# Kernel tuning notes

Measured on AMD Instinct MI355X. Metric: run time of the kernel, lower is better.

The kernel has to match this reference:

```python
import jax, jax.numpy as jnp
import numpy as np

IN_CH, OUT_CH, KS = 64, 128, 3
GRID, DEG = 8, 3
STRIDE, PAD = 1, 1
SIZE = IN_CH * KS * KS            # 576
NCOEF = GRID + DEG                # 11
GRID_RANGE = (-1.0, 1.0)


def _xavier_uniform(key, shape):
    fan_out, fan_in = shape
    a = float(np.sqrt(6.0 / (fan_in + fan_out)))
    return jax.random.uniform(key, shape, minval=-a, maxval=a, dtype=jnp.float32)


def setup_inputs() -> dict:
    key = jax.random.key(0)
    k1, k2, k3 = jax.random.split(key, 3)
    x = jax.random.normal(k1, (8, IN_CH, 32, 32), dtype=jnp.float32)
    # non-trainable knot grid, one row per unfolded feature
    knots = jnp.tile(jnp.linspace(GRID_RANGE[0], GRID_RANGE[1], GRID + 1, dtype=jnp.float32)[None, :], (SIZE, 1))
    coeff = 0.1 * jax.random.normal(k2, (OUT_CH, SIZE, NCOEF), dtype=jnp.float32)
    base_weights = _xavier_uniform(k3, (OUT_CH, SIZE))
    spline_weights = jnp.ones((OUT_CH, SIZE), dtype=jnp.float32)
    return {"x": x, "knots": knots, "coeff": coeff,
            "base_weights": base_weights, "spline_weights": spline_weights}


def bspline_basis(x, grid, k):
    # x: (S, P) evaluation points; grid: (S, G+1) knots. Returns (S, G+k, P).
    h = (grid[:, -1:] - grid[:, :1]) / (grid.shape[1] - 1)
    left = grid[:, :1] - h * jnp.arange(k, 0, -1, dtype=x.dtype)
    right = grid[:, -1:] + h * jnp.arange(1, k + 1, dtype=x.dtype)
    g = jnp.concatenate([left, grid, right], axis=1)  # (S, G+1+2k)
    xe = x[:, None, :]
    B = ((xe >= g[:, :-1, None]) & (xe < g[:, 1:, None])).astype(x.dtype)
    for d in range(1, k + 1):  # de Boor recursion over fixed degree
        B = ((xe - g[:, :-(d + 1), None]) / (g[:, d:-1, None] - g[:, :-(d + 1), None]) * B[:, :-1]
             + (g[:, d + 1:, None] - xe) / (g[:, d + 1:, None] - g[:, 1:-d, None]) * B[:, 1:])
    return B


def _unfold(x):
    # torch F.unfold with channel-major (c, kh, kw) feature ordering
    N, C, H, W = x.shape
    xp = jnp.pad(x, ((0, 0), (0, 0), (PAD, PAD), (PAD, PAD)))
    Hp = (H + 2 * PAD - KS) // STRIDE + 1
    Wp = (W + 2 * PAD - KS) // STRIDE + 1
    patches = jnp.stack([xp[:, :, i:i + STRIDE * Hp:STRIDE, j:j + STRIDE * Wp:STRIDE]
                         for i in range(KS) for j in range(KS)], axis=2)  # (N, C, KS*KS, Hp, Wp)
    L = Hp * Wp
    u = patches.reshape(N, SIZE, L)              # (N, size, L)
    u = jnp.transpose(u, (1, 0, 2)).reshape(SIZE, N * L)  # (size, N*L), col = n*L + l
    return u, Hp, Wp


def reference(x, knots, coeff, base_weights, spline_weights):
    N = x.shape[0]
    u, Hp, Wp = _unfold(x)                                   # (size, P)
    base = base_weights @ jax.nn.silu(u)                     # (Cout, P)
    B = bspline_basis(u, knots, DEG)                         # (size, ncoef, P)
    eff = spline_weights[:, :, None] * coeff                 # (Cout, size, ncoef)
    spl = jnp.einsum('csj,sjp->cp', eff, B)                  # (Cout, P)
    out = (base + spl).reshape(OUT_CH, N, Hp, Wp)
    return jnp.transpose(out, (1, 0, 2, 3))                  # (N, Cout, Hp, Wp)
```

## Files before the change

### kernel.cpp

```cpp
#include <hip/hip_runtime.h>


typedef __attribute__((ext_vector_type(8))) short bf16x8;
typedef __attribute__((ext_vector_type(4))) float f32x4;
typedef __attribute__((ext_vector_type(4))) unsigned short u16x4;

#define WSWZ_BYTES 1769472
#define PART_OFF   WSWZ_BYTES

__device__ __forceinline__ short f2bf(float f) {
    union { float f; unsigned u; } c; c.f = f;
    unsigned r = c.u + 0x7fffu + ((c.u >> 16) & 1u);
    return (short)(r >> 16);
}
__device__ __forceinline__ float bf2f(unsigned short u) {
    union { unsigned u; float f; } c; c.u = ((unsigned)u) << 16;
    return c.f;
}

__global__ void kan_weights(const float* __restrict__ coeff,
                            const float* __restrict__ basew,
                            const float* __restrict__ splw,
                            short* __restrict__ Wswz) {
    __shared__ float coeffL[6336];
    __shared__ float basewL[576];
    __shared__ float splwL[576];
    const int co = blockIdx.x;
    const int t  = threadIdx.x;
    const float* crow = coeff + co * 6336;
    for (int i = t; i < 6336; i += 256) coeffL[i] = crow[i];
    for (int i = t; i < 576; i += 256) {
        basewL[i] = basew[co * 576 + i];
        splwL[i]  = splw[co * 576 + i];
    }
    __syncthreads();
    const int cb = co >> 4, lm = co & 15;
    for (int c = t; c < 864; c += 256) {
        int kk = c >> 2, quad = c & 3;
        int f  = kk / 18;
        int rm = kk - f * 18;
        int tap = rm >> 1, ks = rm & 1;
        bf16x8 pack;
#pragma unroll
        for (int j = 0; j < 8; ++j) {
            int ci = ks * 32 + quad * 8 + j;
            int s  = ci * 9 + tap;
            float v = (f == 0) ? basewL[s] : splwL[s] * coeffL[s * 11 + (f - 1)];
            pack[j] = f2bf(v);
        }
        *(bf16x8*)(Wswz + ((kk * 8 + cb) * 64 + quad * 16 + lm) * 8) = pack;
    }
}

__global__ __launch_bounds__(256, 2)
void kan_gemm(const float* __restrict__ x,
              const short* __restrict__ Wswz,
              float* __restrict__ part) {
    __shared__ unsigned short xs[4 * 64 * 36];
    __shared__ short Bs[3 * 8704];

    const int t    = threadIdx.x;
    const int w    = t >> 6;
    const int l    = t & 63;
    const int lp   = l & 15;
    const int quad = l >> 4;
    const int wm   = w >> 1;
    const int wn   = w & 1;

    const int bz    = blockIdx.x;
    const int fg    = bz & 3;
    const int ptile = bz >> 2;
    const int n     = ptile >> 4;
    const int y0    = (ptile & 15) << 1;

#pragma unroll
    for (int it = 0; it < 8; ++it) {
        int cg = t + it * 256;
        int rr = cg >> 9, ci = (cg >> 3) & 63, q = cg & 7;
        int y  = y0 - 1 + rr;
        f32x4 v = {0.f, 0.f, 0.f, 0.f};
        if (y >= 0 && y < 32)
            v = *(const f32x4*)(x + (((n * 64 + ci) * 32 + y) * 32 + q * 4));
        u16x4 p;
        p.x = (unsigned short)f2bf(v.x); p.y = (unsigned short)f2bf(v.y);
        p.z = (unsigned short)f2bf(v.z); p.w = (unsigned short)f2bf(v.w);
        *(u16x4*)&xs[(rr * 64 + ci) * 36 + q * 4] = p;
    }
    __syncthreads();

    const int f0 = fg * 3;
    for (int it = t; it < 1088; it += 256) {
        int rr  = it / 272;
        int rem = it - rr * 272;
        int xp = rem >> 3, cch = rem & 7, c0 = cch << 3;
        bool interior = (xp >= 1 && xp <= 32);
        bf16x8 packs[3];
#pragma unroll
        for (int j = 0; j < 8; ++j) {
            float v = interior ? bf2f(xs[(rr * 64 + c0 + j) * 36 + (xp - 1)]) : 0.f;
            float silu = v / (1.f + __expf(-v));
            float tt = 4.f * v + 7.f;
            int   i0 = -100;
            float b0 = 0.f, b1 = 0.f, b2 = 0.f, b3 = 0.f;
            if (tt >= 0.f && tt < 14.f) {
                i0 = (int)tt;
                float fr  = tt - (float)i0;
                float omf = 1.f - fr;
                float fr2 = fr * fr, fr3 = fr2 * fr;
                b0 = omf * omf * omf * (1.f / 6.f);
                b1 = (3.f * fr3 - 6.f * fr2 + 4.f) * (1.f / 6.f);
                b2 = (-3.f * fr3 + 3.f * fr2 + 3.f * fr + 1.f) * (1.f / 6.f);
                b3 = fr3 * (1.f / 6.f);
            }
#pragma unroll
            for (int p = 0; p < 3; ++p) {
                int f = f0 + p;
                float val;
                if (f == 0) val = silu;
                else {
                    int jj = f - 1;
                    val = 0.f;
                    val = (jj == i0 - 3) ? b0 : val;
                    val = (jj == i0 - 2) ? b1 : val;
                    val = (jj == i0 - 1) ? b2 : val;
                    val = (jj == i0    ) ? b3 : val;
                }
                packs[p][j] = f2bf(val);
            }
        }
        int pix = rr * 34 + xp;
        int swz = (cch ^ (pix & 7)) << 3;
#pragma unroll
        for (int p = 0; p < 3; ++p)
            *(bf16x8*)&Bs[p * 8704 + pix * 64 + swz] = packs[p];
    }
    __syncthreads();

    f32x4 acc[4][2];
#pragma unroll
    for (int m = 0; m < 4; ++m)
#pragma unroll
        for (int nt = 0; nt < 2; ++nt) {
            f32x4 z = {0.f, 0.f, 0.f, 0.f};
            acc[m][nt] = z;
        }

    const short* Ap = Wswz + (size_t)(f0 * 18) * 4096 + (wm * 4) * 512 + l * 8;

    bf16x8 Abuf[4][4];
#pragma unroll
    for (int s = 0; s < 4; ++s)
#pragma unroll
        for (int m = 0; m < 4; ++m)
            Abuf[s][m] = *(const bf16x8*)(Ap + s * 4096 + m * 512);

#pragma unroll
    for (int u = 0; u < 54; ++u) {
        const int p   = u / 18;
        const int kk  = u - p * 18;
        const int tap = kk >> 1, ks = kk & 1;
        const int dy  = tap / 3;
        const int dx  = tap - dy * 3;
        const int c   = ks * 4 + quad;
        const int s   = u & 3;
        const short* B0 = Bs + p * 8704;

        bf16x8 b[2];
#pragma unroll
        for (int nt = 0; nt < 2; ++nt) {
            int pix = (wn + dy) * 34 + (nt << 4) + lp + dx;
            b[nt] = *(const bf16x8*)&B0[pix * 64 + ((c ^ (pix & 7)) << 3)];
        }
#pragma unroll
        for (int nt = 0; nt < 2; ++nt) {
            acc[0][nt] = __builtin_amdgcn_mfma_f32_16x16x32_bf16(Abuf[s][0], b[nt], acc[0][nt], 0, 0, 0);
            acc[1][nt] = __builtin_amdgcn_mfma_f32_16x16x32_bf16(Abuf[s][1], b[nt], acc[1][nt], 0, 0, 0);
            acc[2][nt] = __builtin_amdgcn_mfma_f32_16x16x32_bf16(Abuf[s][2], b[nt], acc[2][nt], 0, 0, 0);
            acc[3][nt] = __builtin_amdgcn_mfma_f32_16x16x32_bf16(Abuf[s][3], b[nt], acc[3][nt], 0, 0, 0);
        }
#pragma unroll
        for (int m = 0; m < 4; ++m)
            Abuf[s][m] = *(const bf16x8*)(Ap + (u + 4) * 4096 + m * 512);
    }

    float* dst = part + (size_t)fg * 1048576;
#pragma unroll
    for (int m = 0; m < 4; ++m)
#pragma unroll
        for (int nt = 0; nt < 2; ++nt)
#pragma unroll
            for (int r = 0; r < 4; ++r) {
                int co = wm * 64 + m * 16 + quad * 4 + r;
                int y  = y0 + wn;
                int xx = (nt << 4) + lp;
                dst[((size_t)(n * 128 + co) * 32 + y) * 32 + xx] = acc[m][nt][r];
            }
}

__global__ void kan_reduce(const float* __restrict__ part,
                           float* __restrict__ out) {
    int g = blockIdx.x * 256 + threadIdx.x;
    f32x4 a = ((const f32x4*)part)[g];
#pragma unroll
    for (int s = 1; s < 4; ++s)
        a += ((const f32x4*)(part + (size_t)s * 1048576))[g];
    ((f32x4*)out)[g] = a;
}

extern "C" void kernel_launch(void* const* d_in, const int* in_sizes, int n_in,
                              void* d_out, int out_size, void* d_ws, size_t ws_size,
                              hipStream_t stream) {
    const float* x     = (const float*)d_in[0];
    const float* coeff = (const float*)d_in[2];
    const float* basew = (const float*)d_in[3];
    const float* splw  = (const float*)d_in[4];
    float* out = (float*)d_out;

    short* Wswz = (short*)d_ws;
    float* part = (float*)((char*)d_ws + PART_OFF);

    kan_weights<<<128, 256, 0, stream>>>(coeff, basew, splw, Wswz);
    kan_gemm<<<512, 256, 0, stream>>>(x, Wswz, part);
    kan_reduce<<<1024, 256, 0, stream>>>(part, out);
}
```

Before: 107.3 us.

## Split K across warp pairs in GEMM and reduce partial sums through LDS

Each warp pair now splits the K dimension (the two channel halves of each tap) instead of the pixel rows. Every warp covers all four pixel tiles, so each loaded A fragment is reused across four N tiles and global weight loads per MFMA are halved. The software-pipelined A prefetch is removed, and the two K halves are combined through shared memory before the store. The costs are more accumulator registers, two extra barriers for the reduction, and half the warps sitting idle during the final store.

```diff
diff --git a/kernel.cpp b/kernel.cpp
--- a/kernel.cpp
+++ b/kernel.cpp
@@ -65,7 +65,7 @@
     const int lp   = l & 15;
     const int quad = l >> 4;
     const int wm   = w >> 1;
-    const int wn   = w & 1;
+    const int ksw  = w & 1;
 
     const int bz    = blockIdx.x;
     const int fg    = bz & 3;
@@ -136,65 +136,70 @@
     }
     __syncthreads();
 
-    f32x4 acc[4][2];
+    f32x4 acc[4][4];
 #pragma unroll
     for (int m = 0; m < 4; ++m)
 #pragma unroll
-        for (int nt = 0; nt < 2; ++nt) {
+        for (int nt = 0; nt < 4; ++nt) {
             f32x4 z = {0.f, 0.f, 0.f, 0.f};
             acc[m][nt] = z;
         }
 
-    const short* Ap = Wswz + (size_t)(f0 * 18) * 4096 + (wm * 4) * 512 + l * 8;
-
-    bf16x8 Abuf[4][4];
-#pragma unroll
-    for (int s = 0; s < 4; ++s)
+    const short* Abase = Wswz + (size_t)(wm * 4) * 512 + l * 8;
+    const int c = ksw * 4 + quad;
+#pragma unroll
+    for (int p = 0; p < 3; ++p) {
+        const short* B0 = Bs + p * 8704;
+#pragma unroll
+        for (int tap = 0; tap < 9; ++tap) {
+            const int kk = (f0 + p) * 18 + tap * 2 + ksw;
+            const int dy = tap / 3;
+            const int dx = tap - dy * 3;
+            const short* Ak = Abase + (size_t)kk * 4096;
+            bf16x8 a[4], b[4];
+#pragma unroll
+            for (int m = 0; m < 4; ++m)
+                a[m] = *(const bf16x8*)(Ak + m * 512);
+#pragma unroll
+            for (int nt = 0; nt < 4; ++nt) {
+                int pix = ((nt >> 1) + dy) * 34 + ((nt & 1) << 4) + lp + dx;
+                b[nt] = *(const bf16x8*)&B0[pix * 64 + ((c ^ (pix & 7)) << 3)];
+            }
+#pragma unroll
+            for (int m = 0; m < 4; ++m)
+#pragma unroll
+                for (int nt = 0; nt < 4; ++nt)
+                    acc[m][nt] = __builtin_amdgcn_mfma_f32_16x16x32_bf16(a[m], b[nt], acc[m][nt], 0, 0, 0);
+        }
+    }
+
+    __syncthreads();
+    float* red = (float*)Bs;
+    if (ksw == 1) {
 #pragma unroll
         for (int m = 0; m < 4; ++m)
-            Abuf[s][m] = *(const bf16x8*)(Ap + s * 4096 + m * 512);
-
-#pragma unroll
-    for (int u = 0; u < 54; ++u) {
-        const int p   = u / 18;
-        const int kk  = u - p * 18;
-        const int tap = kk >> 1, ks = kk & 1;
-        const int dy  = tap / 3;
-        const int dx  = tap - dy * 3;
-        const int c   = ks * 4 + quad;
-        const int s   = u & 3;
-        const short* B0 = Bs + p * 8704;
-
-        bf16x8 b[2];
-#pragma unroll
-        for (int nt = 0; nt < 2; ++nt) {
-            int pix = (wn + dy) * 34 + (nt << 4) + lp + dx;
-            b[nt] = *(const bf16x8*)&B0[pix * 64 + ((c ^ (pix & 7)) << 3)];
-        }
-#pragma unroll
-        for (int nt = 0; nt < 2; ++nt) {
-            acc[0][nt] = __builtin_amdgcn_mfma_f32_16x16x32_bf16(Abuf[s][0], b[nt], acc[0][nt], 0, 0, 0);
-            acc[1][nt] = __builtin_amdgcn_mfma_f32_16x16x32_bf16(Abuf[s][1], b[nt], acc[1][nt], 0, 0, 0);
-            acc[2][nt] = __builtin_amdgcn_mfma_f32_16x16x32_bf16(Abuf[s][2], b[nt], acc[2][nt], 0, 0, 0);
-            acc[3][nt] = __builtin_amdgcn_mfma_f32_16x16x32_bf16(Abuf[s][3], b[nt], acc[3][nt], 0, 0, 0);
-        }
+#pragma unroll
+            for (int nt = 0; nt < 4; ++nt)
+                *(f32x4*)&red[(((m * 4 + nt) * 128) + wm * 64 + l) * 4] = acc[m][nt];
+    }
+    __syncthreads();
+
+    if (ksw == 0) {
+        float* dst = part + (size_t)fg * 1048576;
 #pragma unroll
         for (int m = 0; m < 4; ++m)
-            Abuf[s][m] = *(const bf16x8*)(Ap + (u + 4) * 4096 + m * 512);
-    }
-
-    float* dst = part + (size_t)fg * 1048576;
-#pragma unroll
-    for (int m = 0; m < 4; ++m)
-#pragma unroll
-        for (int nt = 0; nt < 2; ++nt)
-#pragma unroll
-            for (int r = 0; r < 4; ++r) {
-                int co = wm * 64 + m * 16 + quad * 4 + r;
-                int y  = y0 + wn;
-                int xx = (nt << 4) + lp;
-                dst[((size_t)(n * 128 + co) * 32 + y) * 32 + xx] = acc[m][nt][r];
-            }
+#pragma unroll
+            for (int nt = 0; nt < 4; ++nt) {
+                f32x4 o = acc[m][nt] + *(const f32x4*)&red[(((m * 4 + nt) * 128) + wm * 64 + l) * 4];
+                int y  = y0 + (nt >> 1);
+                int xx = ((nt & 1) << 4) + lp;
+#pragma unroll
+                for (int r = 0; r < 4; ++r) {
+                    int co = wm * 64 + m * 16 + quad * 4 + r;
+                    dst[((size_t)(n * 128 + co) * 32 + y) * 32 + xx] = o[r];
+                }
+            }
+    }
 }
 
 __global__ void kan_reduce(const float* __restrict__ part,
```

Measured after the change: 108.5 us. Within noise of the previous version (+1.1%).
